# Performance work log

Hardware: AMD Instinct MI355X
Metric: run time of the kernel (lower is better)

Reference implementation:

```python
import jax, jax.numpy as jnp
import numpy as np

S = 2048
NODE_DIM = 128
H = 8          # num_heads
C = 32         # num_channels


def setup_inputs() -> dict:
    key = jax.random.key(0)
    ks = jax.random.split(key, 12)
    inv = lambda n: 1.0 / np.sqrt(n)
    inp = {
        "nodes": jax.random.normal(ks[0], (S, NODE_DIM), dtype=jnp.float32),
        "pos": jax.random.uniform(ks[1], (S, 3), dtype=jnp.float32),
        "rot": jax.random.normal(ks[2], (S, 4), dtype=jnp.float32),
        # eqx.nn.Linear weights are (out_features, in_features)
        "w_nodes_kq": jax.random.uniform(ks[3], (H * C * 2, NODE_DIM), minval=-inv(NODE_DIM), maxval=inv(NODE_DIM)),
        "b_nodes_kq": jax.random.uniform(ks[4], (H * C * 2,), minval=-inv(NODE_DIM), maxval=inv(NODE_DIM)),
        "w_pos_kq": jax.random.uniform(ks[5], (H * C * 2, 6), minval=-inv(6), maxval=inv(6)),
        "b_pos_kq": jax.random.uniform(ks[6], (H * C * 2,), minval=-inv(6), maxval=inv(6)),
        "w_rot_kq": jax.random.uniform(ks[7], (H * C * 2, 4), minval=-inv(4), maxval=inv(4)),  # no bias
        "w_values": jax.random.uniform(ks[8], (NODE_DIM * H * 3, NODE_DIM), minval=-inv(NODE_DIM), maxval=inv(NODE_DIM)),
        "b_values": jax.random.uniform(ks[9], (NODE_DIM * H * 3,), minval=-inv(NODE_DIM), maxval=inv(NODE_DIM)),
    }
    return inp


def reference(nodes, pos, rot, w_nodes_kq, b_nodes_kq, w_pos_kq, b_pos_kq,
              w_rot_kq, w_values, b_values):
    seq_len = nodes.shape[0]
    # circular positional features: [S, 6]
    pos_feat = jnp.concatenate([jnp.cos(2 * jnp.pi * pos), jnp.sin(2 * jnp.pi * pos)], axis=-1)

    # values: [S, 3H, node_dim]
    val = (nodes @ w_values.T + b_values).reshape(seq_len, 3 * H, -1)

    # per-source k/q projections, each -> [S, H, C]
    nodes_k, nodes_q = jnp.split((nodes @ w_nodes_kq.T + b_nodes_kq).reshape(seq_len, H, -1), 2, -1)
    pos_k, pos_q = jnp.split((pos_feat @ w_pos_kq.T + b_pos_kq).reshape(seq_len, H, -1), 2, -1)
    rot_k, rot_q = jnp.split((rot @ w_rot_kq.T).reshape(seq_len, H, -1), 2, -1)

    # concat over head axis -> [S, 3H, C]
    k = jnp.concatenate([nodes_k, pos_k, rot_k], axis=-2)
    q = jnp.concatenate([nodes_q, pos_q, rot_q], axis=-2)

    # logits: [S, S, 3H]; square the last H (rotation) heads' sub-logits
    logits = jnp.einsum('ihc,jhc->ijh', k, q)
    logits = logits.at[..., -H:].set(jnp.square(logits[..., -H:]))

    # softmax over j (axis=-2), then weighted sum of values over j and heads
    att = jax.nn.softmax(logits, axis=-2)
    out = jnp.einsum('ijh,jhd->id', att, val)  # [S, node_dim]
    return out
```

## Files before the change

### kernel.cpp

```cpp
#include <hip/hip_runtime.h>
#include <hip/hip_bf16.h>
#include <math.h>

#define SEQ 2048
#define NHEAD 24
#define CDIM 32
#define VDIM 128

typedef short bf16x8 __attribute__((ext_vector_type(8)));
typedef float f32x4 __attribute__((ext_vector_type(4)));

#define L2E 1.44269504088896f
#define SQRT_L2E 1.20112240878645f

#if __has_builtin(__builtin_amdgcn_exp2f)
#define EXP2(x) __builtin_amdgcn_exp2f(x)
#else
#define EXP2(x) exp2f(x)
#endif

__device__ unsigned short g_kkp[(size_t)24 * 128 * 2 * 64 * 8];
__device__ unsigned short g_qv[(size_t)24 * 32 * 24 * 64 * 8];
__device__ unsigned short g_wp[(size_t)224 * 4 * 2 * 64 * 8];
__device__ unsigned short g_np[(size_t)128 * 4 * 2 * 64 * 8];

__device__ __forceinline__ unsigned short f2b(float x) {
  union { float f; unsigned u; } v; v.f = x;
  unsigned r = v.u + 0x7FFF + ((v.u >> 16) & 1);
  return (unsigned short)(r >> 16);
}
__device__ __forceinline__ float b2f(unsigned short u) {
  union { unsigned u32; float f; } x; x.u32 = ((unsigned)u) << 16; return x.f;
}
__device__ __forceinline__ unsigned pk2(float a, float b) {
  __hip_bfloat162 t = __float22bfloat162_rn(float2{a, b});
  union { __hip_bfloat162 h; unsigned u; } c; c.h = t; return c.u;
}
__device__ __forceinline__ unsigned long long pack64(const float* p) {
  return ((unsigned long long)pk2(p[2], p[3]) << 32) | pk2(p[0], p[1]);
}
__device__ __forceinline__ float bperm_f(int srclane, float v) {
  union { float f; int i; } u; u.f = v;
  u.i = __builtin_amdgcn_ds_bpermute(srclane * 4, u.i);
  return u.f;
}
__device__ __forceinline__ void gld16(const unsigned short* g, unsigned short* l) {
  __builtin_amdgcn_global_load_lds(
      (const __attribute__((address_space(1))) unsigned int*)g,
      (__attribute__((address_space(3))) unsigned int*)l, 16, 0, 0);
}

__global__ __launch_bounds__(256) void k_pre(const float* __restrict__ nodes,
                                             const float* __restrict__ w_v,
                                             const float* __restrict__ w_n,
                                             float* __restrict__ out) {
  const int bx = blockIdx.x;
  if (bx < 1024) { out[bx * 256 + threadIdx.x] = 0.f; return; }
  const int bb = bx - 1024;
  const int tid = bb * 256 + threadIdx.x;
  const int fg = tid >> 6, lane = tid & 63;
  const int e0 = (lane >> 4) * 8;
  const float* p;
  unsigned short* dst;
  if (bb < 224) {
    const int colblk = fg >> 2, ks = fg & 3;
    const int ocol = colblk * 16 + (lane & 15);
    const float* src = (ocol < 3072) ? (w_v + (size_t)ocol * 128)
                                     : (w_n + (size_t)(ocol - 3072) * 128);
    p = src + ks * 32 + e0;
    dst = g_wp + (size_t)fg * 1024;
  } else {
    const int fg2 = fg - 224 * 4;
    const int rowblk = fg2 >> 2, ks = fg2 & 3;
    p = nodes + (size_t)(rowblk * 16 + (lane & 15)) * 128 + ks * 32 + e0;
    dst = g_np + (size_t)fg2 * 1024;
  }
  float4 f0 = *(const float4*)p;
  float4 f1 = *(const float4*)(p + 4);
  float ff[8] = {f0.x, f0.y, f0.z, f0.w, f1.x, f1.y, f1.z, f1.w};
  bf16x8 hi, lo;
#pragma unroll
  for (int e = 0; e < 8; ++e) {
    unsigned short h2 = f2b(ff[e]);
    hi[e] = (short)h2;
    lo[e] = (short)f2b(ff[e] - b2f(h2));
  }
  *(bf16x8*)(dst + (size_t)lane * 8) = hi;
  *(bf16x8*)(dst + 512 + (size_t)lane * 8) = lo;
}

__device__ __forceinline__ void repack_store(const unsigned* __restrict__ res,
                                             int oh, int it16, int tx, int head_base) {
#pragma unroll
  for (int t2 = 0; t2 < 2; ++t2) {
    int cid = tx + t2 * 256;
    int hl  = cid >> 7;
    int kq  = (cid >> 6) & 1;
    int row = cid & 63;
    int m = row & 15;
    int ob = hl * 64 + kq * 32 + (row >> 4) * 8;
    bf16x8 hi, lo;
#pragma unroll
    for (int e = 0; e < 8; ++e) {
      unsigned pk = res[(ob + e) * 17 + m];
      hi[e] = (short)(pk >> 16);
      lo[e] = (short)(pk & 0xffff);
    }
    int gh = head_base + oh * 4 + hl;
    if (kq == 0) {
      size_t base = ((size_t)(gh * 128 + it16) * 2) * 512 + (size_t)row * 8;
      *(bf16x8*)(g_kkp + base) = hi;
      *(bf16x8*)(g_kkp + base + 512) = lo;
    } else {
      int jt = it16 >> 2, jb = it16 & 3;
      size_t base = (((size_t)gh * 32 + jt) * 24 + jb * 2) * 512 + (size_t)row * 8;
      *(bf16x8*)(g_qv + base) = hi;
      *(bf16x8*)(g_qv + base + 512) = lo;
    }
  }
}

__global__ __launch_bounds__(256) void k_mid(const float* __restrict__ b_v,
                                             const float* __restrict__ b_n,
                                             const float* __restrict__ pos,
                                             const float* __restrict__ rot,
                                             const float* __restrict__ w_p,
                                             const float* __restrict__ b_p,
                                             const float* __restrict__ w_r) {
  __shared__ __align__(16) char smem[53248];
  const int bx = blockIdx.x;
  const int tx = threadIdx.x;

  if (bx < 1792) {
    const int jt = bx & 31;
    const int bo = bx >> 5;
    const bool is_kq = bo >= 48;
    const float* bsrc = is_kq ? b_n : b_v;
    const int o0b = is_kq ? (bo - 48) * 64 : bo * 64;
    const int w = tx >> 6, lane = tx & 63;
    const int m = lane & 15, quad = lane >> 4;

    unsigned short (*bst)[64][8] = (unsigned short(*)[64][8])smem;
    float (*res)[64][20] = (float(*)[64][20])(smem + 32768);

    const unsigned short* wp = g_wp + ((size_t)bo * 32 + w * 8) * 512 + (size_t)lane * 8;
#pragma unroll
    for (int s = 0; s < 8; ++s)
      gld16(wp + s * 512, &bst[w * 8 + s][0][0]);

    bf16x8 ah[4], al[4];
    const unsigned short* np = g_np + (size_t)(jt * 4 + w) * 4096 + (size_t)lane * 8;
#pragma unroll
    for (int ks = 0; ks < 4; ++ks) {
      ah[ks] = *(const bf16x8*)(np + ks * 1024);
      al[ks] = *(const bf16x8*)(np + ks * 1024 + 512);
    }
    __syncthreads();

    f32x4 C[4];
#pragma unroll
    for (int ob = 0; ob < 4; ++ob) {
      f32x4 acc = {0.f, 0.f, 0.f, 0.f};
#pragma unroll
      for (int ks = 0; ks < 4; ++ks) {
        bf16x8 bh = *(const bf16x8*)&bst[ob * 8 + ks * 2][lane][0];
        bf16x8 bl = *(const bf16x8*)&bst[ob * 8 + ks * 2 + 1][lane][0];
        acc = __builtin_amdgcn_mfma_f32_16x16x32_bf16(ah[ks], bh, acc, 0, 0, 0);
        acc = __builtin_amdgcn_mfma_f32_16x16x32_bf16(al[ks], bh, acc, 0, 0, 0);
        acc = __builtin_amdgcn_mfma_f32_16x16x32_bf16(ah[ks], bl, acc, 0, 0, 0);
      }
      C[ob] = acc;
    }
#pragma unroll
    for (int ob = 0; ob < 4; ++ob) {
      float bias = bsrc[o0b + ob * 16 + m];
#pragma unroll
      for (int r = 0; r < 4; ++r)
        res[w][ob * 16 + m][quad * 4 + r] = C[ob][r] + bias;
    }
    if (!is_kq) {
      const int g = bo >> 1, dbb = (bo & 1) * 4;
      const int jc = w >> 1, khb = (w & 1) * 2;
#pragma unroll
      for (int oct = 0; oct < 2; ++oct) {
        f32x4 v0 = *(const f32x4*)&res[w][quad * 16 + m][oct * 8];
        f32x4 v1 = *(const f32x4*)&res[w][quad * 16 + m][oct * 8 + 4];
        bf16x8 pk;
#pragma unroll
        for (int e = 0; e < 4; ++e) {
          pk[e]     = (short)f2b(v0[e]);
          pk[4 + e] = (short)f2b(v1[e]);
        }
        ((bf16x8*)g_qv)[(((size_t)g * 32 + jt) * 24 + 8 + jc * 8 + dbb + quad) * 64
                        + (khb + oct) * 16 + m] = pk;
      }
    } else {
      const int h = bo - 48;
      {
        bf16x8 hi, lo;
#pragma unroll
        for (int e = 0; e < 8; ++e) {
          float v = res[w][quad * 8 + e][m] * L2E;
          unsigned short h2 = f2b(v);
          hi[e] = (short)h2;
          lo[e] = (short)f2b(v - b2f(h2));
        }
        size_t base = ((size_t)(h * 128 + jt * 4 + w) * 2) * 512 + (size_t)(quad * 16 + m) * 8;
        *(bf16x8*)(g_kkp + base) = hi;
        *(bf16x8*)(g_kkp + base + 512) = lo;
      }
      {
        bf16x8 hi, lo;
#pragma unroll
        for (int e = 0; e < 8; ++e) {
          float v = res[w][32 + quad * 8 + e][m];
          unsigned short h2 = f2b(v);
          hi[e] = (short)h2;
          lo[e] = (short)f2b(v - b2f(h2));
        }
        size_t base = (((size_t)h * 32 + jt) * 24 + w * 2) * 512 + (size_t)(quad * 16 + m) * 8;
        *(bf16x8*)(g_qv + base) = hi;
        *(bf16x8*)(g_qv + base + 512) = lo;
      }
    }
  } else {
    const int r0 = bx - 1792;
    const int it16 = r0 & 127, oh = (r0 >> 7) & 1, br = r0 >> 8;
    const int i0 = it16 * 16;
    unsigned* res = (unsigned*)smem;
    float (*pf_sh)[8] = (float(*)[8])(smem + 17408);
    float (*rr_sh)[4] = (float(*)[4])(smem + 17920);

    if (br == 0) {
      if (tx < 48) {
        int r = tx / 3, t = tx - r * 3;
        float p = pos[(i0 + r) * 3 + t];
        pf_sh[r][t]     = cosf(6.283185307179586f * p);
        pf_sh[r][t + 3] = sinf(6.283185307179586f * p);
      }
    } else {
      if (tx < 64) {
        int r = tx >> 2, t = tx & 3;
        rr_sh[r][t] = rot[(i0 + r) * 4 + t];
      }
    }
    __syncthreads();

    const int og = tx & 63, ig = tx >> 6;
    if (br == 0) {
#pragma unroll
      for (int oo = 0; oo < 4; ++oo) {
        int o = oh * 256 + oo * 64 + og;
        float bb = b_p[o];
        float w0 = w_p[o * 6 + 0], w1 = w_p[o * 6 + 1], w2 = w_p[o * 6 + 2];
        float w3 = w_p[o * 6 + 3], w4 = w_p[o * 6 + 4], w5 = w_p[o * 6 + 5];
        float sc = ((o & 63) < 32) ? L2E : 1.f;
#pragma unroll
        for (int ii = 0; ii < 4; ++ii) {
          int i = ig * 4 + ii;
          float v = bb + pf_sh[i][0] * w0 + pf_sh[i][1] * w1 + pf_sh[i][2] * w2
                       + pf_sh[i][3] * w3 + pf_sh[i][4] * w4 + pf_sh[i][5] * w5;
          v *= sc;
          unsigned short hi = f2b(v);
          unsigned short lo = f2b(v - b2f(hi));
          res[(oo * 64 + og) * 17 + i] = ((unsigned)hi << 16) | lo;
        }
      }
    } else {
#pragma unroll
      for (int oo = 0; oo < 4; ++oo) {
        int o = oh * 256 + oo * 64 + og;
        float w0 = w_r[o * 4 + 0], w1 = w_r[o * 4 + 1], w2 = w_r[o * 4 + 2], w3 = w_r[o * 4 + 3];
        float sc = ((o & 63) < 32) ? SQRT_L2E : 1.f;
#pragma unroll
        for (int ii = 0; ii < 4; ++ii) {
          int i = ig * 4 + ii;
          float v = (rr_sh[i][0] * w0 + rr_sh[i][1] * w1 + rr_sh[i][2] * w2 + rr_sh[i][3] * w3) * sc;
          unsigned short hi = f2b(v);
          unsigned short lo = f2b(v - b2f(hi));
          res[(oo * 64 + og) * 17 + i] = ((unsigned)hi << 16) | lo;
        }
      }
    }
    __syncthreads();
    repack_store(res, oh, it16, tx, 8 + br * 8);
  }
}

__global__ __launch_bounds__(256, 3) void k_attn(float* __restrict__ out) {
  const int it = blockIdx.x;
  const int g  = blockIdx.y;
  const int tx = threadIdx.x;
  const int w = tx >> 6, lane = tx & 63;
  const int quad = lane >> 4, n = lane & 15;
  const int iblk = it * 4 + w;

  __shared__ __align__(16) unsigned short stage[2][24][64][8];
  __shared__ __align__(16) unsigned long long p_lds[4][64][2];

  const bf16x8* kp = (const bf16x8*)g_kkp + (size_t)(g * 128 + iblk) * 2 * 64;
  const bf16x8 khi = kp[lane], klo = kp[64 + lane];

  f32x4 oacc[8];
#pragma unroll
  for (int db = 0; db < 8; ++db)
#pragma unroll
    for (int r = 0; r < 4; ++r) oacc[db][r] = 0.f;

  float m_run = -3.0e38f, l_part = 0.f;
  const bool is_rot = (g >= 16);
  const int pin = (lane & 56) | ((lane ^ (lane >> 3)) & 7);
  const int wrow0 = (quad >> 1) * 16 + n;
  const int wrow1 = wrow0 + 32;
  const int pr0 = (wrow0 & 56) | ((wrow0 ^ (wrow0 >> 3)) & 7);
  const int pr1 = (wrow1 & 56) | ((wrow1 ^ (wrow1 >> 3)) & 7);
  const int whalf = quad & 1;

  const unsigned short* qv = g_qv + ((size_t)g * 32 * 24 + w * 6) * 512 + (size_t)lane * 8;

#define STG(nb)                                          \
  { gld16(qv,             &stage[nb][w * 6 + 0][0][0]);  \
    gld16(qv + 512,       &stage[nb][w * 6 + 1][0][0]);  \
    gld16(qv + 1024,      &stage[nb][w * 6 + 2][0][0]);  \
    gld16(qv + 1536,      &stage[nb][w * 6 + 3][0][0]);  \
    gld16(qv + 2048,      &stage[nb][w * 6 + 4][0][0]);  \
    gld16(qv + 2560,      &stage[nb][w * 6 + 5][0][0]); }

  STG(0)

  bf16x8 a0 = {}, a1 = {};
  bf16x8 vprev[16];

  for (int jt = 0; jt < 32; ++jt) {
    const int buf = jt & 1;
    __syncthreads();

    if (jt) {
#pragma unroll
      for (int db = 0; db < 8; ++db)
        oacc[db] = __builtin_amdgcn_mfma_f32_16x16x32_bf16(a0, vprev[db], oacc[db], 0, 0, 0);
#pragma unroll
      for (int db = 0; db < 8; ++db)
        oacc[db] = __builtin_amdgcn_mfma_f32_16x16x32_bf16(a1, vprev[8 + db], oacc[db], 0, 0, 0);
    }

    qv += 24 * 512;
    if (jt < 31) STG(buf ^ 1)

    const bf16x8* st = (const bf16x8*)&stage[buf][0][0][0];
    f32x4 S[4];
#pragma unroll
    for (int jb = 0; jb < 4; ++jb) {
      bf16x8 qh = st[(jb * 2) * 64 + lane], ql = st[(jb * 2 + 1) * 64 + lane];
      f32x4 a = {0.f, 0.f, 0.f, 0.f};
      a = __builtin_amdgcn_mfma_f32_16x16x32_bf16(qh, khi, a, 0, 0, 0);
      a = __builtin_amdgcn_mfma_f32_16x16x32_bf16(ql, khi, a, 0, 0, 0);
      a = __builtin_amdgcn_mfma_f32_16x16x32_bf16(qh, klo, a, 0, 0, 0);
      S[jb] = a;
    }
    if (is_rot) {
#pragma unroll
      for (int jb = 0; jb < 4; ++jb)
#pragma unroll
        for (int r = 0; r < 4; ++r) S[jb][r] *= S[jb][r];
    }
    float mloc = S[0][0];
#pragma unroll
    for (int jb = 0; jb < 4; ++jb)
#pragma unroll
      for (int r = 0; r < 4; ++r) mloc = fmaxf(mloc, S[jb][r]);
    if (__ballot(mloc > m_run)) {
      float mb = fmaxf(mloc, __shfl_xor(mloc, 16));
      mb = fmaxf(mb, __shfl_xor(mb, 32));
      float m_new = fmaxf(m_run, mb);
      float alpha = EXP2(m_run - m_new);
      m_run = m_new;
      l_part *= alpha;
      f32x4 av;
#pragma unroll
      for (int r = 0; r < 4; ++r) av[r] = bperm_f(quad * 4 + r, alpha);
#pragma unroll
      for (int db = 0; db < 8; ++db) {
        oacc[db][0] *= av[0]; oacc[db][1] *= av[1];
        oacc[db][2] *= av[2]; oacc[db][3] *= av[3];
      }
    }
    float p[4][4];
#pragma unroll
    for (int jb = 0; jb < 4; ++jb)
#pragma unroll
      for (int r = 0; r < 4; ++r) {
        p[jb][r] = EXP2(S[jb][r] - m_run);
        l_part += p[jb][r];
      }
    p_lds[w][pr0][whalf] = pack64(p[0]);
    p_lds[w][pr1][whalf] = pack64(p[1]);
    a0 = *(const bf16x8*)&p_lds[w][pin][0];
    p_lds[w][pr0][whalf] = pack64(p[2]);
    p_lds[w][pr1][whalf] = pack64(p[3]);
    a1 = *(const bf16x8*)&p_lds[w][pin][0];
#pragma unroll
    for (int f = 0; f < 16; ++f) vprev[f] = st[(8 + f) * 64 + lane];
  }
#pragma unroll
  for (int db = 0; db < 8; ++db)
    oacc[db] = __builtin_amdgcn_mfma_f32_16x16x32_bf16(a0, vprev[db], oacc[db], 0, 0, 0);
#pragma unroll
  for (int db = 0; db < 8; ++db)
    oacc[db] = __builtin_amdgcn_mfma_f32_16x16x32_bf16(a1, vprev[8 + db], oacc[db], 0, 0, 0);

  float l = l_part;
  l += __shfl_xor(l, 16);
  l += __shfl_xor(l, 32);
  float linv = 1.f / l;
  f32x4 lv;
#pragma unroll
  for (int r = 0; r < 4; ++r) lv[r] = bperm_f(quad * 4 + r, linv);
  const int ibase = it * 64 + w * 16 + quad * 4;
#pragma unroll
  for (int db = 0; db < 8; ++db)
#pragma unroll
    for (int r = 0; r < 4; ++r)
      atomicAdd(&out[(size_t)(ibase + r) * VDIM + db * 16 + n], oacc[db][r] * lv[r]);
}

extern "C" void kernel_launch(void* const* d_in, const int* in_sizes, int n_in,
                              void* d_out, int out_size, void* d_ws, size_t ws_size,
                              hipStream_t stream) {
  const float* nodes = (const float*)d_in[0];
  const float* pos   = (const float*)d_in[1];
  const float* rot   = (const float*)d_in[2];
  const float* w_n   = (const float*)d_in[3];
  const float* b_n   = (const float*)d_in[4];
  const float* w_p   = (const float*)d_in[5];
  const float* b_p   = (const float*)d_in[6];
  const float* w_r   = (const float*)d_in[7];
  const float* w_v   = (const float*)d_in[8];
  const float* b_v   = (const float*)d_in[9];
  float* out = (float*)d_out;

  k_pre<<<dim3(1024 + 352), 256, 0, stream>>>(nodes, w_v, w_n, out);
  k_mid<<<dim3(1792 + 512), 256, 0, stream>>>(b_v, b_n, pos, rot, w_p, b_p, w_r);
  k_attn<<<dim3(32, NHEAD), 256, 0, stream>>>(out);
}
```

Measured before the change: 163.8 us.

## Replace online softmax max with Cauchy-Schwarz static bound for non-rotation heads

The prologue now computes per-row key norms and a per-head maximum query norm (via atomicMax). The attention kernel uses their product as a fixed upper bound on the logits of the 16 non-rotation heads. That bound seeds the QK accumulator, so the running max, ballot, shuffles and accumulator rescaling leave the inner loop for those heads. The cost is extra prologue work and atomics. It also risks fp32 underflow in exp2 when the bound is much looser than the true row max; rotation heads keep the online softmax.

```diff
diff --git a/kernel.cpp b/kernel.cpp
--- a/kernel.cpp
+++ b/kernel.cpp
@@ -23,6 +23,8 @@
 __device__ unsigned short g_qv[(size_t)24 * 32 * 24 * 64 * 8];
 __device__ unsigned short g_wp[(size_t)224 * 4 * 2 * 64 * 8];
 __device__ unsigned short g_np[(size_t)128 * 4 * 2 * 64 * 8];
+__device__ float g_kn[24 * 2048];
+__device__ unsigned g_qmax[24];
 
 __device__ __forceinline__ unsigned short f2b(float x) {
   union { float f; unsigned u; } v; v.f = x;
@@ -55,7 +57,11 @@
                                              const float* __restrict__ w_n,
                                              float* __restrict__ out) {
   const int bx = blockIdx.x;
-  if (bx < 1024) { out[bx * 256 + threadIdx.x] = 0.f; return; }
+  if (bx < 1024) {
+    if (bx == 0 && threadIdx.x < 24) g_qmax[threadIdx.x] = 0u;
+    out[bx * 256 + threadIdx.x] = 0.f;
+    return;
+  }
   const int bb = bx - 1024;
   const int tid = bb * 256 + threadIdx.x;
   const int fg = tid >> 6, lane = tid & 63;
@@ -222,6 +228,22 @@
         *(bf16x8*)(g_qv + base) = hi;
         *(bf16x8*)(g_qv + base + 512) = lo;
       }
+      if (lane < 16) {
+        float sk = 0.f, sq = 0.f;
+#pragma unroll 8
+        for (int c = 0; c < 32; ++c) {
+          float kv = res[w][c][lane];
+          float qv2 = res[w][32 + c][lane];
+          sk += kv * kv; sq += qv2 * qv2;
+        }
+        g_kn[h * 2048 + jt * 64 + w * 16 + lane] = sqrtf(sk) * (L2E * 1.0001f);
+        float qn = sqrtf(sq) * 1.0001f;
+        qn = fmaxf(qn, __shfl_xor(qn, 1));
+        qn = fmaxf(qn, __shfl_xor(qn, 2));
+        qn = fmaxf(qn, __shfl_xor(qn, 4));
+        qn = fmaxf(qn, __shfl_xor(qn, 8));
+        if (lane == 0) atomicMax(&g_qmax[h], __float_as_uint(qn));
+      }
     }
   } else {
     const int r0 = bx - 1792;
@@ -284,6 +306,26 @@
     }
     __syncthreads();
     repack_store(res, oh, it16, tx, 8 + br * 8);
+    if (br == 0 && tx < 64) {
+      int hl = tx >> 4, i = tx & 15;
+      float sk = 0.f, sq = 0.f;
+#pragma unroll 8
+      for (int c = 0; c < 32; ++c) {
+        unsigned pkk = res[(hl * 64 + c) * 17 + i];
+        unsigned pkq = res[(hl * 64 + 32 + c) * 17 + i];
+        float kv = b2f((unsigned short)(pkk >> 16)) + b2f((unsigned short)(pkk & 0xffff));
+        float qv2 = b2f((unsigned short)(pkq >> 16)) + b2f((unsigned short)(pkq & 0xffff));
+        sk += kv * kv; sq += qv2 * qv2;
+      }
+      int gh = 8 + oh * 4 + hl;
+      g_kn[gh * 2048 + i0 + i] = sqrtf(sk) * 1.0002f;
+      float qn = sqrtf(sq) * 1.0002f;
+      qn = fmaxf(qn, __shfl_xor(qn, 1));
+      qn = fmaxf(qn, __shfl_xor(qn, 2));
+      qn = fmaxf(qn, __shfl_xor(qn, 4));
+      qn = fmaxf(qn, __shfl_xor(qn, 8));
+      if (i == 0) atomicMax(&g_qmax[gh], __float_as_uint(qn));
+    }
   }
 }
 
@@ -307,8 +349,8 @@
 #pragma unroll
     for (int r = 0; r < 4; ++r) oacc[db][r] = 0.f;
 
-  float m_run = -3.0e38f, l_part = 0.f;
   const bool is_rot = (g >= 16);
+  float l_part = 0.f;
   const int pin = (lane & 56) | ((lane ^ (lane >> 3)) & 7);
   const int wrow0 = (quad >> 1) * 16 + n;
   const int wrow1 = wrow0 + 32;
@@ -331,76 +373,120 @@
   bf16x8 a0 = {}, a1 = {};
   bf16x8 vprev[16];
 
-  for (int jt = 0; jt < 32; ++jt) {
-    const int buf = jt & 1;
-    __syncthreads();
-
-    if (jt) {
-#pragma unroll
-      for (int db = 0; db < 8; ++db)
-        oacc[db] = __builtin_amdgcn_mfma_f32_16x16x32_bf16(a0, vprev[db], oacc[db], 0, 0, 0);
-#pragma unroll
-      for (int db = 0; db < 8; ++db)
-        oacc[db] = __builtin_amdgcn_mfma_f32_16x16x32_bf16(a1, vprev[8 + db], oacc[db], 0, 0, 0);
-    }
-
-    qv += 24 * 512;
-    if (jt < 31) STG(buf ^ 1)
-
-    const bf16x8* st = (const bf16x8*)&stage[buf][0][0][0];
-    f32x4 S[4];
-#pragma unroll
-    for (int jb = 0; jb < 4; ++jb) {
-      bf16x8 qh = st[(jb * 2) * 64 + lane], ql = st[(jb * 2 + 1) * 64 + lane];
-      f32x4 a = {0.f, 0.f, 0.f, 0.f};
-      a = __builtin_amdgcn_mfma_f32_16x16x32_bf16(qh, khi, a, 0, 0, 0);
-      a = __builtin_amdgcn_mfma_f32_16x16x32_bf16(ql, khi, a, 0, 0, 0);
-      a = __builtin_amdgcn_mfma_f32_16x16x32_bf16(qh, klo, a, 0, 0, 0);
-      S[jb] = a;
-    }
-    if (is_rot) {
+  if (!is_rot) {
+    const float M = g_kn[g * 2048 + iblk * 16 + n] * __uint_as_float(g_qmax[g]);
+    const f32x4 sInit = {-M, -M, -M, -M};
+    for (int jt = 0; jt < 32; ++jt) {
+      const int buf = jt & 1;
+      __syncthreads();
+      if (jt) {
+#pragma unroll
+        for (int db = 0; db < 8; ++db)
+          oacc[db] = __builtin_amdgcn_mfma_f32_16x16x32_bf16(a0, vprev[db], oacc[db], 0, 0, 0);
+#pragma unroll
+        for (int db = 0; db < 8; ++db)
+          oacc[db] = __builtin_amdgcn_mfma_f32_16x16x32_bf16(a1, vprev[8 + db], oacc[db], 0, 0, 0);
+      }
+      qv += 24 * 512;
+      if (jt < 31) STG(buf ^ 1)
+
+      const bf16x8* st = (const bf16x8*)&stage[buf][0][0][0];
+      f32x4 S[4];
+#pragma unroll
+      for (int jb = 0; jb < 4; ++jb) {
+        bf16x8 qh = st[(jb * 2) * 64 + lane], ql = st[(jb * 2 + 1) * 64 + lane];
+        f32x4 a = sInit;
+        a = __builtin_amdgcn_mfma_f32_16x16x32_bf16(qh, khi, a, 0, 0, 0);
+        a = __builtin_amdgcn_mfma_f32_16x16x32_bf16(ql, khi, a, 0, 0, 0);
+        a = __builtin_amdgcn_mfma_f32_16x16x32_bf16(qh, klo, a, 0, 0, 0);
+        S[jb] = a;
+      }
+      float p[4][4];
 #pragma unroll
       for (int jb = 0; jb < 4; ++jb)
 #pragma unroll
+        for (int r = 0; r < 4; ++r) {
+          p[jb][r] = EXP2(S[jb][r]);
+          l_part += p[jb][r];
+        }
+      p_lds[w][pr0][whalf] = pack64(p[0]);
+      p_lds[w][pr1][whalf] = pack64(p[1]);
+      a0 = *(const bf16x8*)&p_lds[w][pin][0];
+      p_lds[w][pr0][whalf] = pack64(p[2]);
+      p_lds[w][pr1][whalf] = pack64(p[3]);
+      a1 = *(const bf16x8*)&p_lds[w][pin][0];
+#pragma unroll
+      for (int f = 0; f < 16; ++f) vprev[f] = st[(8 + f) * 64 + lane];
+    }
+  } else {
+    float m_run = -3.0e38f;
+    for (int jt = 0; jt < 32; ++jt) {
+      const int buf = jt & 1;
+      __syncthreads();
+      if (jt) {
+#pragma unroll
+        for (int db = 0; db < 8; ++db)
+          oacc[db] = __builtin_amdgcn_mfma_f32_16x16x32_bf16(a0, vprev[db], oacc[db], 0, 0, 0);
+#pragma unroll
+        for (int db = 0; db < 8; ++db)
+          oacc[db] = __builtin_amdgcn_mfma_f32_16x16x32_bf16(a1, vprev[8 + db], oacc[db], 0, 0, 0);
+      }
+      qv += 24 * 512;
+      if (jt < 31) STG(buf ^ 1)
+
+      const bf16x8* st = (const bf16x8*)&stage[buf][0][0][0];
+      f32x4 S[4];
+#pragma unroll
+      for (int jb = 0; jb < 4; ++jb) {
+        bf16x8 qh = st[(jb * 2) * 64 + lane], ql = st[(jb * 2 + 1) * 64 + lane];
+        f32x4 a = {0.f, 0.f, 0.f, 0.f};
+        a = __builtin_amdgcn_mfma_f32_16x16x32_bf16(qh, khi, a, 0, 0, 0);
+        a = __builtin_amdgcn_mfma_f32_16x16x32_bf16(ql, khi, a, 0, 0, 0);
+        a = __builtin_amdgcn_mfma_f32_16x16x32_bf16(qh, klo, a, 0, 0, 0);
+        S[jb] = a;
+      }
+#pragma unroll
+      for (int jb = 0; jb < 4; ++jb)
+#pragma unroll
         for (int r = 0; r < 4; ++r) S[jb][r] *= S[jb][r];
-    }
-    float mloc = S[0][0];
-#pragma unroll
-    for (int jb = 0; jb < 4; ++jb)
-#pragma unroll
-      for (int r = 0; r < 4; ++r) mloc = fmaxf(mloc, S[jb][r]);
-    if (__ballot(mloc > m_run)) {
-      float mb = fmaxf(mloc, __shfl_xor(mloc, 16));
-      mb = fmaxf(mb, __shfl_xor(mb, 32));
-      float m_new = fmaxf(m_run, mb);
-      float alpha = EXP2(m_run - m_new);
-      m_run = m_new;
-      l_part *= alpha;
-      f32x4 av;
-#pragma unroll
-      for (int r = 0; r < 4; ++r) av[r] = bperm_f(quad * 4 + r, alpha);
-#pragma unroll
-      for (int db = 0; db < 8; ++db) {
-        oacc[db][0] *= av[0]; oacc[db][1] *= av[1];
-        oacc[db][2] *= av[2]; oacc[db][3] *= av[3];
-      }
-    }
-    float p[4][4];
-#pragma unroll
-    for (int jb = 0; jb < 4; ++jb)
-#pragma unroll
-      for (int r = 0; r < 4; ++r) {
-        p[jb][r] = EXP2(S[jb][r] - m_run);
-        l_part += p[jb][r];
-      }
-    p_lds[w][pr0][whalf] = pack64(p[0]);
-    p_lds[w][pr1][whalf] = pack64(p[1]);
-    a0 = *(const bf16x8*)&p_lds[w][pin][0];
-    p_lds[w][pr0][whalf] = pack64(p[2]);
-    p_lds[w][pr1][whalf] = pack64(p[3]);
-    a1 = *(const bf16x8*)&p_lds[w][pin][0];
-#pragma unroll
-    for (int f = 0; f < 16; ++f) vprev[f] = st[(8 + f) * 64 + lane];
+      float mloc = S[0][0];
+#pragma unroll
+      for (int jb = 0; jb < 4; ++jb)
+#pragma unroll
+        for (int r = 0; r < 4; ++r) mloc = fmaxf(mloc, S[jb][r]);
+      if (__ballot(mloc > m_run)) {
+        float mb = fmaxf(mloc, __shfl_xor(mloc, 16));
+        mb = fmaxf(mb, __shfl_xor(mb, 32));
+        float m_new = fmaxf(m_run, mb);
+        float alpha = EXP2(m_run - m_new);
+        m_run = m_new;
+        l_part *= alpha;
+        f32x4 av;
+#pragma unroll
+        for (int r = 0; r < 4; ++r) av[r] = bperm_f(quad * 4 + r, alpha);
+#pragma unroll
+        for (int db = 0; db < 8; ++db) {
+          oacc[db][0] *= av[0]; oacc[db][1] *= av[1];
+          oacc[db][2] *= av[2]; oacc[db][3] *= av[3];
+        }
+      }
+      float p[4][4];
+#pragma unroll
+      for (int jb = 0; jb < 4; ++jb)
+#pragma unroll
+        for (int r = 0; r < 4; ++r) {
+          p[jb][r] = EXP2(S[jb][r] - m_run);
+          l_part += p[jb][r];
+        }
+      p_lds[w][pr0][whalf] = pack64(p[0]);
+      p_lds[w][pr1][whalf] = pack64(p[1]);
+      a0 = *(const bf16x8*)&p_lds[w][pin][0];
+      p_lds[w][pr0][whalf] = pack64(p[2]);
+      p_lds[w][pr1][whalf] = pack64(p[3]);
+      a1 = *(const bf16x8*)&p_lds[w][pin][0];
+#pragma unroll
+      for (int f = 0; f < 16; ++f) vprev[f] = st[(8 + f) * 64 + lane];
+    }
   }
 #pragma unroll
   for (int db = 0; db < 8; ++db)
```

After: 166.7 us. Within noise of the previous version (+1.8%).
